# Performance work log

Hardware: AMD Instinct MI355X
Metric: run time of the kernel (lower is better)

## Reference

```python
import jax, jax.numpy as jnp
import numpy as np

EPS = 1e-5
K_NN = 16

def _lin1d(x, W, b):
    # 1x1 Conv1d: x (B,C,N) -> (B,O,N)
    return jnp.einsum('oc,bcn->bon', W, x) + b[None, :, None]

def _lin2d(x, W, b):
    # 1x1 Conv2d: x (B,C,N,K) -> (B,O,N,K)
    return jnp.einsum('oc,bcnk->bonk', W, x) + b[None, :, None, None]

def _bn2d(x, gamma, beta):
    # train-mode BatchNorm2d over (B, N, K) per channel
    mean = jnp.mean(x, axis=(0, 2, 3), keepdims=True)
    var = jnp.var(x, axis=(0, 2, 3), keepdims=True)
    xh = (x - mean) * jax.lax.rsqrt(var + EPS)
    return gamma[None, :, None, None] * xh + beta[None, :, None, None]

def _knn_idx(pq, ps, k):
    # pq (B,3,N), ps (B,3,M) -> idx (B,N,K) of k nearest support points
    d2 = (jnp.sum(pq * pq, axis=1)[:, :, None]
          + jnp.sum(ps * ps, axis=1)[:, None, :]
          - 2.0 * jnp.einsum('bcn,bcm->bnm', pq, ps))
    _, idx = jax.lax.top_k(-d2, k)
    return idx

def _group(x, idx):
    # x (B,C,M), idx (B,N,K) -> (B,C,N,K)
    return jnp.take_along_axis(x[:, :, None, :], idx[:, None, :, :], axis=3)

def setup_inputs() -> dict:
    key = jax.random.key(0)
    ks = jax.random.split(key, 20)
    B, C, D, N, M, H = 4, 128, 64, 2048, 2048, 256
    s = lambda k, shape, scale: (jax.random.normal(k, shape, dtype=jnp.float32) * scale)
    return {
        'pq': s(ks[0], (B, 3, N), 1.0),
        'fq': s(ks[1], (B, C, N), 1.0),
        'ps': s(ks[2], (B, 3, M), 1.0),
        'fs': s(ks[3], (B, C, M), 1.0),
        'Wq': s(ks[4], (D, C), 0.05), 'bq': jnp.zeros((D,), jnp.float32),
        'Wk': s(ks[5], (D, C), 0.05), 'bk': jnp.zeros((D,), jnp.float32),
        'Wv': s(ks[6], (D, C), 0.05), 'bv': jnp.zeros((D,), jnp.float32),
        'Wp1': s(ks[7], (D, 3), 0.2), 'bp1': jnp.zeros((D,), jnp.float32),
        'gp': jnp.ones((D,), jnp.float32), 'btp': jnp.zeros((D,), jnp.float32),
        'Wp2': s(ks[8], (D, D), 0.05), 'bp2': jnp.zeros((D,), jnp.float32),
        'Wa1': s(ks[9], (H, D), 0.05), 'ba1': jnp.zeros((H,), jnp.float32),
        'ga': jnp.ones((H,), jnp.float32), 'bta': jnp.zeros((H,), jnp.float32),
        'Wa2': s(ks[10], (D, H), 0.05), 'ba2': jnp.zeros((D,), jnp.float32),
        'We': s(ks[11], (C, D), 0.05), 'be': jnp.zeros((C,), jnp.float32),
    }

def reference(pq, fq, ps, fs, Wq, bq, Wk, bk, Wv, bv,
              Wp1, bp1, gp, btp, Wp2, bp2,
              Wa1, ba1, ga, bta, Wa2, ba2, We, be):
    identity = fq
    q = _lin1d(fq, Wq, bq)          # (B,D,N)
    k = _lin1d(fs, Wk, bk)          # (B,D,M)
    v = _lin1d(fs, Wv, bv)          # (B,D,M)
    idx = _knn_idx(pq, ps, K_NN)    # (B,N,K)
    key_g = _group(k, idx)          # (B,D,N,K)
    qk_rel = q[:, :, :, None] - key_g
    pos_rel = pq[:, :, :, None] - _group(ps, idx)  # (B,3,N,K)
    # pos_mlp: conv-bn-relu-conv
    pe = _lin2d(pos_rel, Wp1, bp1)
    pe = jax.nn.relu(_bn2d(pe, gp, btp))
    pe = _lin2d(pe, Wp2, bp2)       # (B,D,N,K)
    # attn_mlp: conv-bn-relu-conv
    a = _lin2d(qk_rel + pe, Wa1, ba1)
    a = jax.nn.relu(_bn2d(a, ga, bta))
    a = _lin2d(a, Wa2, ba2)         # (B,D,N,K)
    attn = jax.nn.softmax(a, axis=-1)
    val = _group(v, idx) + pe       # (B,D,N,K)
    agg = jnp.einsum('bcnk,bcnk->bcn', attn, val)
    return _lin1d(agg, We, be) + identity
```

## Files before the change

kernel.cpp:

```cpp
#include <hip/hip_runtime.h>
#include <stdint.h>

#define NN 2048
#define MM 2048
#define NSAMP 131072

typedef float  fv4 __attribute__((ext_vector_type(4)));
typedef short  bfv8 __attribute__((ext_vector_type(8)));
typedef short  bfv4 __attribute__((ext_vector_type(4)));
typedef unsigned short u16;
typedef unsigned long long u64;

__device__ inline u16 f2bf(float x){
  unsigned u = __float_as_uint(x);
  return (u16)((u + 0x7FFFu + ((u>>16)&1u)) >> 16);
}
__device__ inline float bf2f(u16 u){ return __uint_as_float(((unsigned)u)<<16); }
#define MFMA16 __builtin_amdgcn_mfma_f32_16x16x32_bf16

__global__ __launch_bounds__(256) void k_prep(
    const float* __restrict__ Wq, const float* __restrict__ Wk, const float* __restrict__ Wv,
    const float* __restrict__ Wp2, const float* __restrict__ Wa2, const float* __restrict__ We,
    const float* __restrict__ ps,
    u16* __restrict__ Wqbf, u16* __restrict__ Wkbf, u16* __restrict__ Wvbf,
    u16* __restrict__ Wp2bf, u16* __restrict__ Wa2bf, u16* __restrict__ Webf,
    fv4* __restrict__ psP) {
  int gid = blockIdx.x * 256 + threadIdx.x;
  if (gid < 8192)  { Wqbf[gid] = f2bf(Wq[gid]); Wkbf[gid] = f2bf(Wk[gid]);
                     Wvbf[gid] = f2bf(Wv[gid]); Webf[gid] = f2bf(We[gid]); }
  if (gid < 4096)  Wp2bf[gid] = f2bf(Wp2[gid]);
  if (gid < 16384) Wa2bf[gid] = f2bf(Wa2[gid]);
  if (gid < 8192)  { int b = gid >> 11, m = gid & 2047;
    float x = ps[(b*3+0)*MM + m], y = ps[(b*3+1)*MM + m], z = ps[(b*3+2)*MM + m];
    fv4 p; p.x = x; p.y = y; p.z = z; p.w = x*x + y*y + z*z;
    psP[gid] = p; }
}

__global__ __launch_bounds__(256) void k_qkv(
    const float* __restrict__ fq, const float* __restrict__ fs,
    const u16* __restrict__ Wqbf, const u16* __restrict__ Wkbf, const u16* __restrict__ Wvbf,
    const float* __restrict__ bq, const float* __restrict__ bk, const float* __restrict__ bv,
    float* __restrict__ qT, float* __restrict__ kT, float* __restrict__ vT) {
  __shared__ u16 tile[2][32 * 136];
  int bid = blockIdx.x;
  int b = bid >> 6, p0 = (bid & 63) * 32;
  int t = threadIdx.x;
  int w = t >> 6, l = t & 63, lq = l >> 4, ln = l & 15;
  {
    int cq = t >> 3, n4 = (t & 7) * 4;
    #pragma unroll
    for (int it = 0; it < 4; ++it) {
      int c = it * 32 + cq;
      fv4 vq = *(const fv4*)&fq[(b*128 + c)*2048 + p0 + n4];
      fv4 vs = *(const fv4*)&fs[(b*128 + c)*2048 + p0 + n4];
      #pragma unroll
      for (int j = 0; j < 4; ++j) {
        tile[0][(n4 + j)*136 + c] = f2bf(vq[j]);
        tile[1][(n4 + j)*136 + c] = f2bf(vs[j]);
      }
    }
  }
  bfv8 A[3][4];
  #pragma unroll
  for (int mat = 0; mat < 3; ++mat) {
    const u16* W = mat == 0 ? Wqbf : (mat == 1 ? Wkbf : Wvbf);
    #pragma unroll
    for (int kk = 0; kk < 4; ++kk)
      A[mat][kk] = *(const bfv8*)(W + (w*16 + ln)*128 + kk*32 + lq*8);
  }
  __syncthreads();
  fv4 acc[3][2];
  #pragma unroll
  for (int mat = 0; mat < 3; ++mat) {
    const u16* tl = tile[mat == 0 ? 0 : 1];
    #pragma unroll
    for (int nt = 0; nt < 2; ++nt) {
      fv4 a = {0.f,0.f,0.f,0.f};
      #pragma unroll
      for (int kk = 0; kk < 4; ++kk) {
        bfv8 bb = *(const bfv8*)&tl[(nt*16 + ln)*136 + kk*32 + lq*8];
        a = MFMA16(A[mat][kk], bb, a, 0, 0, 0);
      }
      acc[mat][nt] = a;
    }
  }
  #pragma unroll
  for (int mat = 0; mat < 3; ++mat) {
    float* dst = mat == 0 ? qT : (mat == 1 ? kT : vT);
    const float* bia = mat == 0 ? bq : (mat == 1 ? bk : bv);
    fv4 bq4 = *(const fv4*)&bia[w*16 + lq*4];
    #pragma unroll
    for (int nt = 0; nt < 2; ++nt) {
      fv4 o = acc[mat][nt] + bq4;
      *(fv4*)&dst[(b*NN + p0 + nt*16 + ln)*64 + w*16 + lq*4] = o;
    }
  }
}

__global__ __launch_bounds__(256) void k_knn(
    const float* __restrict__ pq, const fv4* __restrict__ psP,
    int* __restrict__ idxb, float* __restrict__ posPart) {
  __shared__ u64 list[4][512];
  __shared__ u64 win[4][16];
  __shared__ int cnt[4];
  __shared__ float sacc[4][9];

  const int t = threadIdx.x, w = t >> 6, lane = t & 63;
  const int qi = blockIdx.x * 4 + w;
  const int b = qi >> 11, n = qi & 2047;
  const float* pqb = pq + b * 3 * NN;
  const fv4* psb = psP + b * 2048;
  const float qx = pqb[n], qy = pqb[NN + n], qz = pqb[2 * NN + n];
  const float qq = qx * qx + qy * qy + qz * qz;

  unsigned key[32];
  unsigned bkey = 0xFFFFFFFFu; unsigned bj = 0;
  #pragma unroll
  for (int j = 0; j < 32; ++j) {
    fv4 P = psb[lane + 64*j];
    float d2 = qq + P.w - 2.f * (qx * P.x + qy * P.y + qz * P.z);
    unsigned bu = __float_as_uint(d2);
    bu = (bu & 0x80000000u) ? ~bu : (bu | 0x80000000u);
    key[j] = bu;
    if (bu < bkey) { bkey = bu; bj = (unsigned)j; }
  }
  u64 e = (((u64)bkey) << 32) | (unsigned)(lane + 64*(int)bj);

  #pragma unroll
  for (int k = 2; k <= 64; k <<= 1) {
    #pragma unroll
    for (int j = k >> 1; j > 0; j >>= 1) {
      u64 x = __shfl_xor(e, j, 64);
      u64 lo = e < x ? e : x, hi = e < x ? x : e;
      bool up = ((lane & k) == 0);
      bool takeLo = (((lane & j) == 0) == up);
      e = takeLo ? lo : hi;
    }
  }
  const u64 thr = __shfl(e, 15, 64);
  const unsigned T32 = (unsigned)(thr >> 32);

  if (lane == 0) cnt[w] = 0;
  #pragma unroll
  for (int j = 0; j < 32; ++j) {
    if (key[j] <= T32) {
      int p = atomicAdd(&cnt[w], 1);
      if (p < 512) list[w][p] = (((u64)key[j]) << 32) | (unsigned)(lane + 64*j);
    }
  }
  const int C = *(volatile int*)&cnt[w];

  u64 myWin = 0;
  if (C <= 64) {
    u64 v = (lane < C) ? list[w][lane] : ~0ULL;
    #pragma unroll
    for (int k = 2; k <= 64; k <<= 1) {
      #pragma unroll
      for (int j = k >> 1; j > 0; j >>= 1) {
        u64 x = __shfl_xor(v, j, 64);
        u64 lo = v < x ? v : x, hi = v < x ? x : v;
        bool up = ((lane & k) == 0);
        bool takeLo = (((lane & j) == 0) == up);
        v = takeLo ? lo : hi;
      }
    }
    myWin = v;
  } else if (C <= 128) {
    u64 e0 = list[w][lane];
    u64 e1 = (64 + lane < C) ? list[w][64 + lane] : ~0ULL;
    #pragma unroll
    for (unsigned k = 2; k <= 128; k <<= 1) {
      #pragma unroll
      for (unsigned j = k >> 1; j > 0; j >>= 1) {
        if (j < 64) {
          u64 x0 = __shfl_xor(e0, (int)j, 64);
          u64 x1 = __shfl_xor(e1, (int)j, 64);
          bool lower = ((lane & j) == 0);
          bool up0 = (k == 128) ? true : ((lane & k) == 0);
          bool up1 = (k == 128) ? true : ((k == 64) ? false : ((lane & k) == 0));
          e0 = (lower == up0) ? (e0 < x0 ? e0 : x0) : (e0 < x0 ? x0 : e0);
          e1 = (lower == up1) ? (e1 < x1 ? e1 : x1) : (e1 < x1 ? x1 : e1);
        } else {
          u64 lo = e0 < e1 ? e0 : e1, hi = e0 < e1 ? e1 : e0;
          e0 = lo; e1 = hi;
        }
      }
    }
    myWin = e0;
  } else {
    int Cc = C > 512 ? 512 : C;
    for (int i = lane; i < 512; i += 64)
      if (i >= Cc) list[w][i] = ~0ULL;
    for (int r = 0; r < 16; ++r) {
      u64 mv = ~0ULL;
      #pragma unroll
      for (int s5 = 0; s5 < 8; ++s5) {
        u64 x = list[w][s5*64 + lane];
        mv = x < mv ? x : mv;
      }
      #pragma unroll
      for (int off = 1; off <= 32; off <<= 1) {
        u64 x = __shfl_xor(mv, off, 64);
        mv = x < mv ? x : mv;
      }
      #pragma unroll
      for (int s5 = 0; s5 < 8; ++s5)
        if (list[w][s5*64 + lane] == mv) list[w][s5*64 + lane] = ~0ULL;
      if (lane == 0) win[w][r] = mv;
    }
    if (lane < 16) myWin = win[w][lane];
  }

  if (lane < 16) {
    unsigned m = (unsigned)(myWin & 0xFFFFFFFFu);
    idxb[qi * 16 + lane] = (int)m;
    fv4 P = psb[m];
    float r0 = qx - P.x, r1 = qy - P.y, r2 = qz - P.z;
    float s[9];
    s[0] = r0; s[1] = r1; s[2] = r2;
    s[3] = r0*r0; s[4] = r0*r1; s[5] = r0*r2;
    s[6] = r1*r1; s[7] = r1*r2; s[8] = r2*r2;
    #pragma unroll
    for (int off = 1; off <= 8; off <<= 1)
      #pragma unroll
      for (int i = 0; i < 9; ++i) s[i] += __shfl_xor(s[i], off, 64);
    if (lane == 0)
      #pragma unroll
      for (int i = 0; i < 9; ++i) sacc[w][i] = s[i];
  }
  __syncthreads();
  if (t < 9) posPart[blockIdx.x * 12 + t]
      = sacc[0][t] + sacc[1][t] + sacc[2][t] + sacc[3][t];
}

__global__ __launch_bounds__(256) void k_posfinal(
    const float* __restrict__ Wp1, const float* __restrict__ bp1,
    const float* __restrict__ gp, const float* __restrict__ btp,
    const float* __restrict__ posPart, float* __restrict__ Wp1f, float* __restrict__ bp1f) {
  __shared__ float red[4][9];
  __shared__ float st[9];
  int t = threadIdx.x;
  int w = t >> 6, lane = t & 63;
  float s[9];
  #pragma unroll
  for (int i = 0; i < 9; ++i) s[i] = 0.f;
  #pragma unroll
  for (int it = 0; it < 8; ++it) {
    const float* p = posPart + (it * 256 + t) * 12;
    fv4 a = *(const fv4*)p;
    fv4 b4 = *(const fv4*)(p + 4);
    float c8 = p[8];
    s[0]+=a.x; s[1]+=a.y; s[2]+=a.z; s[3]+=a.w;
    s[4]+=b4.x; s[5]+=b4.y; s[6]+=b4.z; s[7]+=b4.w;
    s[8]+=c8;
  }
  #pragma unroll
  for (int off = 32; off > 0; off >>= 1)
    #pragma unroll
    for (int i = 0; i < 9; ++i) s[i] += __shfl_xor(s[i], off, 64);
  if (lane == 0)
    #pragma unroll
    for (int i = 0; i < 9; ++i) red[w][i] = s[i];
  __syncthreads();
  if (t < 9) st[t] = red[0][t] + red[1][t] + red[2][t] + red[3][t];
  __syncthreads();
  if (t < 64) {
    int d = t;
    const float invN = 1.f / (float)NSAMP;
    float m0 = st[0]*invN, m1 = st[1]*invN, m2 = st[2]*invN;
    float C00 = st[3]*invN - m0*m0, C01 = st[4]*invN - m0*m1, C02 = st[5]*invN - m0*m2;
    float C11 = st[6]*invN - m1*m1, C12 = st[7]*invN - m1*m2, C22 = st[8]*invN - m2*m2;
    float w0 = Wp1[d*3], w1 = Wp1[d*3+1], w2 = Wp1[d*3+2];
    float mean = w0*m0 + w1*m1 + w2*m2 + bp1[d];
    float var = w0*w0*C00 + w1*w1*C11 + w2*w2*C22 + 2.f*(w0*w1*C01 + w0*w2*C02 + w1*w2*C12);
    float scale = gp[d] * rsqrtf(var + 1e-5f);
    Wp1f[d*3]   = scale * w0;
    Wp1f[d*3+1] = scale * w1;
    Wp1f[d*3+2] = scale * w2;
    bp1f[d] = btp[d] + scale * (bp1[d] - mean);
  }
}

__global__ __launch_bounds__(256) void k_ystats(
    const float* __restrict__ pq, const float* __restrict__ ps,
    const float* __restrict__ qT, const float* __restrict__ kT,
    const int* __restrict__ idxb,
    const float* __restrict__ Wp1f, const float* __restrict__ bp1f,
    const u16* __restrict__ Wp2bf, const float* __restrict__ bp2,
    float* __restrict__ Gpart, float* __restrict__ ySumPart) {
  __shared__ __align__(16) unsigned char smem[21760];
  u16*   hp   = (u16*)smem;
  u16*   y2   = (u16*)(smem + 9216);
  float* r3   = (float*)(smem + 18432);
  float* qc   = (float*)(smem + 19200);
  int*   idxA = (int*)(smem + 20224);
  float* sWp1 = (float*)(smem + 20480);
  float* sbp1 = (float*)(smem + 21248);
  float* sbp2 = (float*)(smem + 21504);

  const int t = threadIdx.x;
  const int w = t >> 6, l = t & 63, lq = l >> 4, ln = l & 15;
  const int d0 = 16*w + lq*4;

  if (t < 192) sWp1[t] = Wp1f[t];
  if (t < 64){ sbp1[t] = bp1f[t]; sbp2[t] = bp2[t]; }

  bfv8 Ape[2];
  #pragma unroll
  for (int kk = 0; kk < 2; ++kk)
    Ape[kk] = *(const bfv8*)(Wp2bf + (16*w + ln)*64 + kk*32 + lq*8);

  fv4 gacc[4];
  #pragma unroll
  for (int nt = 0; nt < 4; ++nt) gacc[nt] = (fv4){0.f,0.f,0.f,0.f};
  float ys[4] = {0.f, 0.f, 0.f, 0.f};
  __syncthreads();

  for (int ch = 0; ch < 2; ++ch) {
    const int p0 = blockIdx.x * 8 + ch * 4;
    const int b  = p0 >> 11;
    const int bN = b * 2048;
    if (t < 64) idxA[t] = idxb[p0*16 + t];
    qc[t] = qT[(p0 + (t>>6))*64 + (t & 63)];
    __syncthreads();
    if (t < 192) { int c = t >> 6, s = t & 63; int n = (p0 + (s>>4)) & 2047;
      r3[c*64 + s] = pq[(b*3+c)*NN + n] - ps[(b*3+c)*MM + idxA[s]]; }
    __syncthreads();
    { int s = t >> 2, iq = t & 3;
      float r0 = r3[s], r1 = r3[64+s], r2 = r3[128+s];
      u16 tmp[16];
      #pragma unroll
      for (int e = 0; e < 16; ++e) { int i = iq*16 + e;
        float v = sbp1[i] + sWp1[i*3]*r0 + sWp1[i*3+1]*r1 + sWp1[i*3+2]*r2;
        tmp[e] = f2bf(fmaxf(v, 0.f)); }
      *(bfv8*)&hp[s*72 + iq*16]     = *(const bfv8*)&tmp[0];
      *(bfv8*)&hp[s*72 + iq*16 + 8] = *(const bfv8*)&tmp[8];
    }
    __syncthreads();
    {
      fv4 pe[4];
      #pragma unroll
      for (int nt = 0; nt < 4; ++nt) {
        fv4 acc = {0.f,0.f,0.f,0.f};
        #pragma unroll
        for (int kk = 0; kk < 2; ++kk) {
          bfv8 bb = *(const bfv8*)&hp[(nt*16 + ln)*72 + kk*32 + lq*8];
          acc = MFMA16(Ape[kk], bb, acc, 0, 0, 0);
        }
        pe[nt] = acc;
      }
      fv4 bp2q = *(const fv4*)&sbp2[d0];
      #pragma unroll
      for (int nt = 0; nt < 4; ++nt) {
        int s = nt*16 + ln;
        int mi = idxA[s];
        fv4 kg = *(const fv4*)(kT + (bN + mi)*64 + d0);
        fv4 qv = *(const fv4*)&qc[nt*64 + d0];
        fv4 yv = qv - kg + pe[nt] + bp2q;
        #pragma unroll
        for (int r = 0; r < 4; ++r) { y2[(d0 + r)*72 + s] = f2bf(yv[r]); ys[r] += yv[r]; }
      }
    }
    __syncthreads();
    #pragma unroll
    for (int kk = 0; kk < 2; ++kk) {
      bfv8 aa = *(const bfv8*)&y2[(16*w + ln)*72 + kk*32 + lq*8];
      #pragma unroll
      for (int nt = 0; nt < 4; ++nt) {
        bfv8 bb = *(const bfv8*)&y2[(nt*16 + ln)*72 + kk*32 + lq*8];
        gacc[nt] = MFMA16(aa, bb, gacc[nt], 0, 0, 0);
      }
    }
    __syncthreads();
  }
  #pragma unroll
  for (int nt = 0; nt < 4; ++nt)
    #pragma unroll
    for (int r = 0; r < 4; ++r)
      Gpart[blockIdx.x*4096 + (16*w + lq*4 + r)*64 + nt*16 + ln] = gacc[nt][r];
  #pragma unroll
  for (int off = 1; off <= 8; off <<= 1) {
    #pragma unroll
    for (int r = 0; r < 4; ++r) ys[r] += __shfl_xor(ys[r], off, 64);
  }
  if (ln == 0) {
    #pragma unroll
    for (int r = 0; r < 4; ++r) ySumPart[blockIdx.x*64 + d0 + r] = ys[r];
  }
}

__global__ __launch_bounds__(256) void k_gred(
    const float* __restrict__ Gpart, const float* __restrict__ ySumPart,
    float* __restrict__ G, float* __restrict__ ySum) {
  __shared__ float red[256];
  int bid = blockIdx.x, t = threadIdx.x;
  int tj = t & 63, st = t >> 6;
  if (bid < 64) {
    int j = bid * 64 + tj;
    float s = 0.f;
    for (int p = st * 256; p < st * 256 + 256; ++p)
      s += Gpart[p*4096 + j];
    red[st * 64 + tj] = s;
    __syncthreads();
    if (t < 64)
      G[bid * 64 + t] = red[t] + red[64 + t] + red[128 + t] + red[192 + t];
  } else {
    float s = 0.f;
    for (int p = st * 256; p < st * 256 + 256; ++p)
      s += ySumPart[p*64 + tj];
    red[st * 64 + tj] = s;
    __syncthreads();
    if (t < 64)
      ySum[t] = red[t] + red[64 + t] + red[128 + t] + red[192 + t];
  }
}

__global__ __launch_bounds__(256) void k_attnfinal(
    const float* __restrict__ Wa1, const float* __restrict__ ba1,
    const float* __restrict__ ga, const float* __restrict__ bta,
    const float* __restrict__ ySum, const float* __restrict__ G,
    u16* __restrict__ Wa1fbf, float* __restrict__ ba1f) {
  __shared__ float red[256];
  __shared__ float mu[64];
  __shared__ float sc[1];
  int h = blockIdx.x, t = threadIdx.x;
  const float invN = 1.f / (float)NSAMP;
  if (t < 64) mu[t] = ySum[t] * invN;
  __syncthreads();
  float acc = 0.f;
  #pragma unroll
  for (int e = 0; e < 16; ++e) {
    int pi = t*16 + e, i = pi >> 6, j = pi & 63;
    float cov = G[pi]*invN - mu[i]*mu[j];
    acc += Wa1[h*64 + i] * Wa1[h*64 + j] * cov;
  }
  red[t] = acc;
  __syncthreads();
  for (int s = 128; s > 0; s >>= 1) { if (t < s) red[t] += red[t + s]; __syncthreads(); }
  float var = red[0];
  __syncthreads();
  red[t] = (t < 64) ? Wa1[h*64 + t] * mu[t] : 0.f;
  __syncthreads();
  for (int s = 128; s > 0; s >>= 1) { if (t < s) red[t] += red[t + s]; __syncthreads(); }
  if (t == 0) {
    float mean  = red[0] + ba1[h];
    float scale = ga[h] * rsqrtf(var + 1e-5f);
    sc[0] = scale;
    ba1f[h] = bta[h] + scale * (ba1[h] - mean);
  }
  __syncthreads();
  if (t < 64) Wa1fbf[h*64 + t] = f2bf(sc[0] * Wa1[h*64 + t]);
}

__global__ __launch_bounds__(256, 4) void k_main(
    const float* __restrict__ pq, const float* __restrict__ ps,
    const float* __restrict__ qT, const float* __restrict__ kT, const float* __restrict__ vT,
    const int* __restrict__ idxb,
    const float* __restrict__ Wp1f, const float* __restrict__ bp1f,
    const u16* __restrict__ Wp2bf, const float* __restrict__ bp2,
    const u16* __restrict__ Wa1fbf, const float* __restrict__ ba1f,
    const u16* __restrict__ Wa2bf, const float* __restrict__ ba2,
    u16* __restrict__ aggbf) {
  __shared__ __align__(16) unsigned char smem[37120];
  u16*   hp   = (u16*)smem;
  u16*   ylds = (u16*)(smem + 9216);
  u16*   ha   = (u16*)smem;
  float* r3   = (float*)(smem + 33792);
  float* qc   = (float*)(smem + 34560);
  int*   idxA = (int*)(smem + 35584);
  float* sWp1 = (float*)(smem + 35840);
  float* sbp1 = (float*)(smem + 36608);
  float* sbp2 = (float*)(smem + 36864);

  const int t = threadIdx.x;
  const int w = t >> 6, l = t & 63, lq = l >> 4, ln = l & 15;
  const int d0 = 16*w + lq*4;
  const int p0 = blockIdx.x * 4;
  const int b  = p0 >> 11;
  const int bN = b * 2048;

  if (t < 192) sWp1[t] = Wp1f[t];
  if (t < 64){ sbp1[t] = bp1f[t]; sbp2[t] = bp2[t]; }
  if (t < 64) idxA[t] = idxb[p0*16 + t];
  qc[t] = qT[(p0 + (t>>6))*64 + (t & 63)];
  __syncthreads();

  if (t < 192) { int c = t >> 6, s = t & 63; int n = (p0 + (s>>4)) & 2047;
    r3[c*64 + s] = pq[(b*3+c)*NN + n] - ps[(b*3+c)*MM + idxA[s]]; }
  __syncthreads();

  { int s = t >> 2, iq = t & 3;
    float r0 = r3[s], r1 = r3[64+s], r2 = r3[128+s];
    u16 tmp[16];
    #pragma unroll
    for (int e = 0; e < 16; ++e) { int i = iq*16 + e;
      float v = sbp1[i] + sWp1[i*3]*r0 + sWp1[i*3+1]*r1 + sWp1[i*3+2]*r2;
      tmp[e] = f2bf(fmaxf(v, 0.f)); }
    *(bfv8*)&hp[s*72 + iq*16]     = *(const bfv8*)&tmp[0];
    *(bfv8*)&hp[s*72 + iq*16 + 8] = *(const bfv8*)&tmp[8];
  }
  __syncthreads();

  u16 vp[4][4];
  {
    bfv8 Ape[2];
    #pragma unroll
    for (int kk = 0; kk < 2; ++kk)
      Ape[kk] = *(const bfv8*)(Wp2bf + (16*w + ln)*64 + kk*32 + lq*8);
    fv4 pe[4];
    #pragma unroll
    for (int nt = 0; nt < 4; ++nt) {
      fv4 acc = {0.f,0.f,0.f,0.f};
      #pragma unroll
      for (int kk = 0; kk < 2; ++kk) {
        bfv8 bb = *(const bfv8*)&hp[(nt*16 + ln)*72 + kk*32 + lq*8];
        acc = MFMA16(Ape[kk], bb, acc, 0, 0, 0);
      }
      pe[nt] = acc;
    }
    fv4 bp2q = *(const fv4*)&sbp2[d0];
    #pragma unroll
    for (int nt = 0; nt < 4; ++nt) {
      int s = nt*16 + ln;
      int mi = idxA[s];
      fv4 kg = *(const fv4*)(kT + (bN + mi)*64 + d0);
      fv4 vg = *(const fv4*)(vT + (bN + mi)*64 + d0);
      fv4 qv = *(const fv4*)&qc[nt*64 + d0];
      fv4 pv = pe[nt] + bp2q;
      fv4 yv = qv - kg + pv;
      fv4 vv = vg + pv;
      u16 yp[4];
      #pragma unroll
      for (int r = 0; r < 4; ++r) { yp[r] = f2bf(yv[r]); vp[nt][r] = f2bf(vv[r]); }
      *(bfv4*)&ylds[s*72 + d0] = *(const bfv4*)yp;
    }
  }
  __syncthreads();

  bfv8 yb0[4], yb1[4];
  #pragma unroll
  for (int nt = 0; nt < 4; ++nt) {
    int s = nt*16 + ln;
    yb0[nt] = *(const bfv8*)&ylds[s*72 + lq*8];
    yb1[nt] = *(const bfv8*)&ylds[s*72 + 32 + lq*8];
  }
  __syncthreads();

  {
    bfv8 A1[4][2];
    #pragma unroll
    for (int mt = 0; mt < 4; ++mt)
      #pragma unroll
      for (int kk = 0; kk < 2; ++kk)
        A1[mt][kk] = *(const bfv8*)(Wa1fbf + (64*w + mt*16 + ln)*64 + kk*32 + lq*8);
    #pragma unroll
    for (int nt = 0; nt < 4; ++nt) {
      int s = nt*16 + ln;
      #pragma unroll
      for (int mt = 0; mt < 4; ++mt) {
        fv4 acc = {0.f,0.f,0.f,0.f};
        acc = MFMA16(A1[mt][0], yb0[nt], acc, 0, 0, 0);
        acc = MFMA16(A1[mt][1], yb1[nt], acc, 0, 0, 0);
        int h0 = 64*w + mt*16 + lq*4;
        fv4 bq = *(const fv4*)&ba1f[h0];
        u16 hv[4];
        #pragma unroll
        for (int r = 0; r < 4; ++r) hv[r] = f2bf(fmaxf(acc[r] + bq[r], 0.f));
        *(bfv4*)&ha[s*264 + h0] = *(const bfv4*)hv;
      }
    }
  }
  __syncthreads();

  fv4 acc2[4];
  #pragma unroll
  for (int nt = 0; nt < 4; ++nt) acc2[nt] = (fv4){0.f,0.f,0.f,0.f};
  {
    #pragma unroll
    for (int kk = 0; kk < 8; ++kk) {
      bfv8 A2 = *(const bfv8*)(Wa2bf + (16*w + ln)*256 + kk*32 + lq*8);
      #pragma unroll
      for (int nt = 0; nt < 4; ++nt) {
        bfv8 bb = *(const bfv8*)&ha[(nt*16 + ln)*264 + kk*32 + lq*8];
        acc2[nt] = MFMA16(A2, bb, acc2[nt], 0, 0, 0);
      }
    }
  }
  const fv4 ba2q = *(const fv4*)&ba2[d0];
  #pragma unroll
  for (int nt = 0; nt < 4; ++nt) {
    fv4 a = acc2[nt] + ba2q;
    fv4 m = a;
    #pragma unroll
    for (int off = 1; off <= 8; off <<= 1)
      #pragma unroll
      for (int r = 0; r < 4; ++r) m[r] = fmaxf(m[r], __shfl_xor(m[r], off, 16));
    fv4 ee, num;
    #pragma unroll
    for (int r = 0; r < 4; ++r) {
      ee[r] = __expf(a[r] - m[r]);
      num[r] = ee[r] * bf2f(vp[nt][r]);
    }
    fv4 sum = ee;
    #pragma unroll
    for (int off = 1; off <= 8; off <<= 1)
      #pragma unroll
      for (int r = 0; r < 4; ++r) {
        sum[r] += __shfl_xor(sum[r], off, 16);
        num[r] += __shfl_xor(num[r], off, 16);
      }
    if (ln == 0) {
      u16 o[4];
      #pragma unroll
      for (int r = 0; r < 4; ++r) o[r] = f2bf(num[r] / sum[r]);
      *(bfv4*)&aggbf[(u64)(p0 + nt)*64 + d0] = *(const bfv4*)o;
    }
  }
}

__global__ __launch_bounds__(256) void k_epi(
    const u16* __restrict__ aggbf, const u16* __restrict__ Webf,
    const float* __restrict__ be, const float* __restrict__ fq,
    float* __restrict__ out) {
  const int t = threadIdx.x;
  const int w = t >> 6, l = t & 63, lq = l >> 4, ln = l & 15;
  const int P0 = blockIdx.x * 16;
  const int b  = P0 >> 11;
  const int n0 = P0 & 2047;
  bfv8 EA[2][2];
  #pragma unroll
  for (int mt = 0; mt < 2; ++mt)
    #pragma unroll
    for (int kk = 0; kk < 2; ++kk)
      EA[mt][kk] = *(const bfv8*)(Webf + ((w*2 + mt)*16 + ln)*64 + kk*32 + lq*8);
  const u16* bp = aggbf + (P0 + ln)*64;
  bfv8 b0 = *(const bfv8*)(bp + lq*8);
  bfv8 b1 = *(const bfv8*)(bp + 32 + lq*8);
  fv4 eacc[2];
  #pragma unroll
  for (int mt = 0; mt < 2; ++mt) {
    fv4 a = {0.f,0.f,0.f,0.f};
    a = MFMA16(EA[mt][0], b0, a, 0, 0, 0);
    a = MFMA16(EA[mt][1], b1, a, 0, 0, 0);
    eacc[mt] = a;
  }
  #pragma unroll
  for (int mt = 0; mt < 2; ++mt) {
    int c0 = (w*2 + mt)*16 + lq*4;
    fv4 bev = *(const fv4*)&be[c0];
    #pragma unroll
    for (int r = 0; r < 4; ++r) {
      int c = c0 + r;
      int o = (b*128 + c)*2048 + n0 + ln;
      out[o] = eacc[mt][r] + bev[r] + fq[o];
    }
  }
}

extern "C" void kernel_launch(void* const* d_in, const int* in_sizes, int n_in,
                              void* d_out, int out_size, void* d_ws, size_t ws_size,
                              hipStream_t stream) {
  (void)in_sizes; (void)n_in; (void)out_size; (void)ws_size;
  const float* pq  = (const float*)d_in[0];
  const float* fq  = (const float*)d_in[1];
  const float* ps  = (const float*)d_in[2];
  const float* fs  = (const float*)d_in[3];
  const float* Wq  = (const float*)d_in[4];  const float* bq  = (const float*)d_in[5];
  const float* Wk  = (const float*)d_in[6];  const float* bk  = (const float*)d_in[7];
  const float* Wv  = (const float*)d_in[8];  const float* bv  = (const float*)d_in[9];
  const float* Wp1 = (const float*)d_in[10]; const float* bp1 = (const float*)d_in[11];
  const float* gp  = (const float*)d_in[12]; const float* btp = (const float*)d_in[13];
  const float* Wp2 = (const float*)d_in[14]; const float* bp2 = (const float*)d_in[15];
  const float* Wa1 = (const float*)d_in[16]; const float* ba1 = (const float*)d_in[17];
  const float* ga  = (const float*)d_in[18]; const float* bta = (const float*)d_in[19];
  const float* Wa2 = (const float*)d_in[20]; const float* ba2 = (const float*)d_in[21];
  const float* We  = (const float*)d_in[22]; const float* be  = (const float*)d_in[23];
  float* ws = (float*)d_ws;
  float* qT    = ws;
  float* kT    = ws + 524288;
  float* vT    = ws + 1048576;
  u16*   aggbf = (u16*)(ws + 1572864);
  int*   idxb  = (int*)(ws + 1835008);
  u16*   Wqbf  = (u16*)(ws + 1966080);
  u16*   Wkbf  = (u16*)(ws + 1970176);
  u16*   Wvbf  = (u16*)(ws + 1974272);
  u16*   Webf  = (u16*)(ws + 1978368);
  fv4*   psP   = (fv4*)(ws + 1982464);
  float* Wp1f  = ws + 2015232;
  float* bp1f  = ws + 2015424;
  float* ba1f  = ws + 2015488;
  float* G     = ws + 2015744;
  float* ySum  = ws + 2019840;
  float* ySumP = ws + 2019904;
  u16*   Wp2bf  = (u16*)(ws + 2085440);
  u16*   Wa2bf  = (u16*)(ws + 2087488);
  u16*   Wa1fbf = (u16*)(ws + 2095680);
  float* posPart = ws + 2103872;
  float* Gpart   = ws + 2128448;
  float* out   = (float*)d_out;

  k_prep<<<64, 256, 0, stream>>>(Wq, Wk, Wv, Wp2, Wa2, We, ps,
                                 Wqbf, Wkbf, Wvbf, Wp2bf, Wa2bf, Webf, psP);
  k_qkv<<<256, 256, 0, stream>>>(fq, fs, Wqbf, Wkbf, Wvbf, bq, bk, bv, qT, kT, vT);
  k_knn<<<2048, 256, 0, stream>>>(pq, psP, idxb, posPart);
  k_posfinal<<<1, 256, 0, stream>>>(Wp1, bp1, gp, btp, posPart, Wp1f, bp1f);
  k_ystats<<<1024, 256, 0, stream>>>(pq, ps, qT, kT, idxb, Wp1f, bp1f, Wp2bf, bp2,
                                     Gpart, ySumP);
  k_gred<<<65, 256, 0, stream>>>(Gpart, ySumP, G, ySum);
  k_attnfinal<<<256, 256, 0, stream>>>(Wa1, ba1, ga, bta, ySum, G, Wa1fbf, ba1f);
  k_main<<<2048, 256, 0, stream>>>(pq, ps, qT, kT, vT, idxb, Wp1f, bp1f, Wp2bf, bp2,
                                   Wa1fbf, ba1f, Wa2bf, ba2, aggbf);
  k_epi<<<512, 256, 0, stream>>>(aggbf, Webf, be, fq, out);
}
```

Baseline: 229.9 us.

## Fuse epilogue projection into main attention kernel with per-block point loop

The main kernel now handles 16 points per block in a loop of four 4-point chunks. It keeps the attention aggregate in shared memory and applies the output projection plus residual directly, so the separate epilogue kernel and the global agg buffer are gone. Weight fragments (Wp2, Wa1, biases) are loaded into registers once per block and reused across the chunks. In exchange the grid shrinks to 512 blocks, shared memory grows, and launch bounds drop to 3 blocks per SM, which lowers occupancy and parallelism.

```diff
diff --git a/kernel.cpp b/kernel.cpp
--- a/kernel.cpp
+++ b/kernel.cpp
@@ -452,7 +452,7 @@
   if (t < 64) Wa1fbf[h*64 + t] = f2bf(sc[0] * Wa1[h*64 + t]);
 }
 
-__global__ __launch_bounds__(256, 4) void k_main(
+__global__ __launch_bounds__(256, 3) void k_main(
     const float* __restrict__ pq, const float* __restrict__ ps,
     const float* __restrict__ qT, const float* __restrict__ kT, const float* __restrict__ vT,
     const int* __restrict__ idxb,
@@ -460,122 +460,117 @@
     const u16* __restrict__ Wp2bf, const float* __restrict__ bp2,
     const u16* __restrict__ Wa1fbf, const float* __restrict__ ba1f,
     const u16* __restrict__ Wa2bf, const float* __restrict__ ba2,
-    u16* __restrict__ aggbf) {
-  __shared__ __align__(16) unsigned char smem[37120];
+    const u16* __restrict__ Webf, const float* __restrict__ be,
+    const float* __restrict__ fq,
+    float* __restrict__ out) {
+  __shared__ __align__(16) unsigned char smem[48640];
   u16*   hp   = (u16*)smem;
-  u16*   ylds = (u16*)(smem + 9216);
   u16*   ha   = (u16*)smem;
-  float* r3   = (float*)(smem + 33792);
-  float* qc   = (float*)(smem + 34560);
-  int*   idxA = (int*)(smem + 35584);
-  float* sWp1 = (float*)(smem + 35840);
-  float* sbp1 = (float*)(smem + 36608);
-  float* sbp2 = (float*)(smem + 36864);
+  u16*   ylds = (u16*)(smem + 33792);
+  float* r3   = (float*)(smem + 43008);
+  float* qc   = (float*)(smem + 43776);
+  int*   idxA = (int*)(smem + 44800);
+  float* sWp1 = (float*)(smem + 45056);
+  float* sbp1 = (float*)(smem + 45824);
+  u16*   aggL = (u16*)(smem + 46336);
 
   const int t = threadIdx.x;
   const int w = t >> 6, l = t & 63, lq = l >> 4, ln = l & 15;
   const int d0 = 16*w + lq*4;
-  const int p0 = blockIdx.x * 4;
-  const int b  = p0 >> 11;
+  const int P0 = blockIdx.x * 16;
+  const int b  = P0 >> 11;
   const int bN = b * 2048;
 
   if (t < 192) sWp1[t] = Wp1f[t];
-  if (t < 64){ sbp1[t] = bp1f[t]; sbp2[t] = bp2[t]; }
-  if (t < 64) idxA[t] = idxb[p0*16 + t];
-  qc[t] = qT[(p0 + (t>>6))*64 + (t & 63)];
-  __syncthreads();
-
-  if (t < 192) { int c = t >> 6, s = t & 63; int n = (p0 + (s>>4)) & 2047;
-    r3[c*64 + s] = pq[(b*3+c)*NN + n] - ps[(b*3+c)*MM + idxA[s]]; }
-  __syncthreads();
-
-  { int s = t >> 2, iq = t & 3;
-    float r0 = r3[s], r1 = r3[64+s], r2 = r3[128+s];
-    u16 tmp[16];
-    #pragma unroll
-    for (int e = 0; e < 16; ++e) { int i = iq*16 + e;
-      float v = sbp1[i] + sWp1[i*3]*r0 + sWp1[i*3+1]*r1 + sWp1[i*3+2]*r2;
-      tmp[e] = f2bf(fmaxf(v, 0.f)); }
-    *(bfv8*)&hp[s*72 + iq*16]     = *(const bfv8*)&tmp[0];
-    *(bfv8*)&hp[s*72 + iq*16 + 8] = *(const bfv8*)&tmp[8];
-  }
-  __syncthreads();
-
-  u16 vp[4][4];
-  {
-    bfv8 Ape[2];
+  if (t < 64) sbp1[t] = bp1f[t];
+
+  bfv8 Ape[2], A1[4][2];
+  #pragma unroll
+  for (int kk = 0; kk < 2; ++kk)
+    Ape[kk] = *(const bfv8*)(Wp2bf + (16*w + ln)*64 + kk*32 + lq*8);
+  #pragma unroll
+  for (int mt = 0; mt < 4; ++mt)
     #pragma unroll
     for (int kk = 0; kk < 2; ++kk)
-      Ape[kk] = *(const bfv8*)(Wp2bf + (16*w + ln)*64 + kk*32 + lq*8);
-    fv4 pe[4];
-    #pragma unroll
-    for (int nt = 0; nt < 4; ++nt) {
-      fv4 acc = {0.f,0.f,0.f,0.f};
-      #pragma unroll
-      for (int kk = 0; kk < 2; ++kk) {
-        bfv8 bb = *(const bfv8*)&hp[(nt*16 + ln)*72 + kk*32 + lq*8];
-        acc = MFMA16(Ape[kk], bb, acc, 0, 0, 0);
-      }
-      pe[nt] = acc;
-    }
-    fv4 bp2q = *(const fv4*)&sbp2[d0];
+      A1[mt][kk] = *(const bfv8*)(Wa1fbf + (64*w + mt*16 + ln)*64 + kk*32 + lq*8);
+  fv4 bq1[4];
+  #pragma unroll
+  for (int mt = 0; mt < 4; ++mt)
+    bq1[mt] = *(const fv4*)&ba1f[64*w + mt*16 + lq*4];
+  const fv4 ba2q = *(const fv4*)&ba2[d0];
+  const fv4 bp2q = *(const fv4*)&bp2[d0];
+
+  for (int ch = 0; ch < 4; ++ch) {
+    const int p0 = P0 + ch * 4;
+    if (t < 64) idxA[t] = idxb[p0*16 + t];
+    qc[t] = qT[(p0 + (t>>6))*64 + (t & 63)];
+    __syncthreads();
+    if (t < 192) { int c = t >> 6, s = t & 63; int n = (p0 + (s>>4)) & 2047;
+      r3[c*64 + s] = pq[(b*3+c)*NN + n] - ps[(b*3+c)*MM + idxA[s]]; }
+    __syncthreads();
+    { int s = t >> 2, iq = t & 3;
+      float r0 = r3[s], r1 = r3[64+s], r2 = r3[128+s];
+      u16 tmp[16];
+      #pragma unroll
+      for (int e = 0; e < 16; ++e) { int i = iq*16 + e;
+        float v = sbp1[i] + sWp1[i*3]*r0 + sWp1[i*3+1]*r1 + sWp1[i*3+2]*r2;
+        tmp[e] = f2bf(fmaxf(v, 0.f)); }
+      *(bfv8*)&hp[s*72 + iq*16]     = *(const bfv8*)&tmp[0];
+      *(bfv8*)&hp[s*72 + iq*16 + 8] = *(const bfv8*)&tmp[8];
+    }
+    __syncthreads();
+    u16 vp[4][4];
+    {
+      fv4 pe[4];
+      #pragma unroll
+      for (int nt = 0; nt < 4; ++nt) {
+        fv4 acc = {0.f,0.f,0.f,0.f};
+        #pragma unroll
+        for (int kk = 0; kk < 2; ++kk) {
+          bfv8 bb = *(const bfv8*)&hp[(nt*16 + ln)*72 + kk*32 + lq*8];
+          acc = MFMA16(Ape[kk], bb, acc, 0, 0, 0);
+        }
+        pe[nt] = acc;
+      }
+      #pragma unroll
+      for (int nt = 0; nt < 4; ++nt) {
+        int s = nt*16 + ln;
+        int mi = idxA[s];
+        fv4 kg = *(const fv4*)(kT + (bN + mi)*64 + d0);
+        fv4 vg = *(const fv4*)(vT + (bN + mi)*64 + d0);
+        fv4 qv = *(const fv4*)&qc[nt*64 + d0];
+        fv4 pv = pe[nt] + bp2q;
+        fv4 yv = qv - kg + pv;
+        fv4 vv = vg + pv;
+        u16 yp[4];
+        #pragma unroll
+        for (int r = 0; r < 4; ++r) { yp[r] = f2bf(yv[r]); vp[nt][r] = f2bf(vv[r]); }
+        *(bfv4*)&ylds[s*72 + d0] = *(const bfv4*)yp;
+      }
+    }
+    __syncthreads();
     #pragma unroll
     for (int nt = 0; nt < 4; ++nt) {
       int s = nt*16 + ln;
-      int mi = idxA[s];
-      fv4 kg = *(const fv4*)(kT + (bN + mi)*64 + d0);
-      fv4 vg = *(const fv4*)(vT + (bN + mi)*64 + d0);
-      fv4 qv = *(const fv4*)&qc[nt*64 + d0];
-      fv4 pv = pe[nt] + bp2q;
-      fv4 yv = qv - kg + pv;
-      fv4 vv = vg + pv;
-      u16 yp[4];
-      #pragma unroll
-      for (int r = 0; r < 4; ++r) { yp[r] = f2bf(yv[r]); vp[nt][r] = f2bf(vv[r]); }
-      *(bfv4*)&ylds[s*72 + d0] = *(const bfv4*)yp;
-    }
-  }
-  __syncthreads();
-
-  bfv8 yb0[4], yb1[4];
-  #pragma unroll
-  for (int nt = 0; nt < 4; ++nt) {
-    int s = nt*16 + ln;
-    yb0[nt] = *(const bfv8*)&ylds[s*72 + lq*8];
-    yb1[nt] = *(const bfv8*)&ylds[s*72 + 32 + lq*8];
-  }
-  __syncthreads();
-
-  {
-    bfv8 A1[4][2];
-    #pragma unroll
-    for (int mt = 0; mt < 4; ++mt)
-      #pragma unroll
-      for (int kk = 0; kk < 2; ++kk)
-        A1[mt][kk] = *(const bfv8*)(Wa1fbf + (64*w + mt*16 + ln)*64 + kk*32 + lq*8);
-    #pragma unroll
-    for (int nt = 0; nt < 4; ++nt) {
-      int s = nt*16 + ln;
+      bfv8 yb0 = *(const bfv8*)&ylds[s*72 + lq*8];
+      bfv8 yb1 = *(const bfv8*)&ylds[s*72 + 32 + lq*8];
       #pragma unroll
       for (int mt = 0; mt < 4; ++mt) {
         fv4 acc = {0.f,0.f,0.f,0.f};
-        acc = MFMA16(A1[mt][0], yb0[nt], acc, 0, 0, 0);
-        acc = MFMA16(A1[mt][1], yb1[nt], acc, 0, 0, 0);
+        acc = MFMA16(A1[mt][0], yb0, acc, 0, 0, 0);
+        acc = MFMA16(A1[mt][1], yb1, acc, 0, 0, 0);
         int h0 = 64*w + mt*16 + lq*4;
-        fv4 bq = *(const fv4*)&ba1f[h0];
+        fv4 bq = bq1[mt];
         u16 hv[4];
         #pragma unroll
         for (int r = 0; r < 4; ++r) hv[r] = f2bf(fmaxf(acc[r] + bq[r], 0.f));
         *(bfv4*)&ha[s*264 + h0] = *(const bfv4*)hv;
       }
     }
-  }
-  __syncthreads();
-
-  fv4 acc2[4];
-  #pragma unroll
-  for (int nt = 0; nt < 4; ++nt) acc2[nt] = (fv4){0.f,0.f,0.f,0.f};
-  {
+    __syncthreads();
+    fv4 acc2[4];
+    #pragma unroll
+    for (int nt = 0; nt < 4; ++nt) acc2[nt] = (fv4){0.f,0.f,0.f,0.f};
     #pragma unroll
     for (int kk = 0; kk < 8; ++kk) {
       bfv8 A2 = *(const bfv8*)(Wa2bf + (16*w + ln)*256 + kk*32 + lq*8);
@@ -585,74 +580,66 @@
         acc2[nt] = MFMA16(A2, bb, acc2[nt], 0, 0, 0);
       }
     }
-  }
-  const fv4 ba2q = *(const fv4*)&ba2[d0];
-  #pragma unroll
-  for (int nt = 0; nt < 4; ++nt) {
-    fv4 a = acc2[nt] + ba2q;
-    fv4 m = a;
-    #pragma unroll
-    for (int off = 1; off <= 8; off <<= 1)
-      #pragma unroll
-      for (int r = 0; r < 4; ++r) m[r] = fmaxf(m[r], __shfl_xor(m[r], off, 16));
-    fv4 ee, num;
-    #pragma unroll
-    for (int r = 0; r < 4; ++r) {
-      ee[r] = __expf(a[r] - m[r]);
-      num[r] = ee[r] * bf2f(vp[nt][r]);
-    }
-    fv4 sum = ee;
-    #pragma unroll
-    for (int off = 1; off <= 8; off <<= 1)
+    #pragma unroll
+    for (int nt = 0; nt < 4; ++nt) {
+      fv4 a = acc2[nt] + ba2q;
+      fv4 m = a;
+      #pragma unroll
+      for (int off = 1; off <= 8; off <<= 1)
+        #pragma unroll
+        for (int r = 0; r < 4; ++r) m[r] = fmaxf(m[r], __shfl_xor(m[r], off, 16));
+      fv4 ee, num;
       #pragma unroll
       for (int r = 0; r < 4; ++r) {
-        sum[r] += __shfl_xor(sum[r], off, 16);
-        num[r] += __shfl_xor(num[r], off, 16);
-      }
-    if (ln == 0) {
-      u16 o[4];
-      #pragma unroll
-      for (int r = 0; r < 4; ++r) o[r] = f2bf(num[r] / sum[r]);
-      *(bfv4*)&aggbf[(u64)(p0 + nt)*64 + d0] = *(const bfv4*)o;
-    }
-  }
-}
-
-__global__ __launch_bounds__(256) void k_epi(
-    const u16* __restrict__ aggbf, const u16* __restrict__ Webf,
-    const float* __restrict__ be, const float* __restrict__ fq,
-    float* __restrict__ out) {
-  const int t = threadIdx.x;
-  const int w = t >> 6, l = t & 63, lq = l >> 4, ln = l & 15;
-  const int P0 = blockIdx.x * 16;
-  const int b  = P0 >> 11;
-  const int n0 = P0 & 2047;
-  bfv8 EA[2][2];
-  #pragma unroll
-  for (int mt = 0; mt < 2; ++mt)
-    #pragma unroll
-    for (int kk = 0; kk < 2; ++kk)
-      EA[mt][kk] = *(const bfv8*)(Webf + ((w*2 + mt)*16 + ln)*64 + kk*32 + lq*8);
-  const u16* bp = aggbf + (P0 + ln)*64;
-  bfv8 b0 = *(const bfv8*)(bp + lq*8);
-  bfv8 b1 = *(const bfv8*)(bp + 32 + lq*8);
-  fv4 eacc[2];
-  #pragma unroll
-  for (int mt = 0; mt < 2; ++mt) {
-    fv4 a = {0.f,0.f,0.f,0.f};
-    a = MFMA16(EA[mt][0], b0, a, 0, 0, 0);
-    a = MFMA16(EA[mt][1], b1, a, 0, 0, 0);
-    eacc[mt] = a;
-  }
-  #pragma unroll
-  for (int mt = 0; mt < 2; ++mt) {
-    int c0 = (w*2 + mt)*16 + lq*4;
-    fv4 bev = *(const fv4*)&be[c0];
-    #pragma unroll
-    for (int r = 0; r < 4; ++r) {
-      int c = c0 + r;
-      int o = (b*128 + c)*2048 + n0 + ln;
-      out[o] = eacc[mt][r] + bev[r] + fq[o];
+        ee[r] = __expf(a[r] - m[r]);
+        num[r] = ee[r] * bf2f(vp[nt][r]);
+      }
+      fv4 sum = ee;
+      #pragma unroll
+      for (int off = 1; off <= 8; off <<= 1)
+        #pragma unroll
+        for (int r = 0; r < 4; ++r) {
+          sum[r] += __shfl_xor(sum[r], off, 16);
+          num[r] += __shfl_xor(num[r], off, 16);
+        }
+      if (ln == 0) {
+        u16 o[4];
+        #pragma unroll
+        for (int r = 0; r < 4; ++r) o[r] = f2bf(num[r] / sum[r]);
+        *(bfv4*)&aggL[(ch*4 + nt)*72 + d0] = *(const bfv4*)o;
+      }
+    }
+    __syncthreads();
+  }
+  {
+    const int n0 = P0 & 2047;
+    bfv8 EA[2][2];
+    #pragma unroll
+    for (int mt = 0; mt < 2; ++mt)
+      #pragma unroll
+      for (int kk = 0; kk < 2; ++kk)
+        EA[mt][kk] = *(const bfv8*)(Webf + ((w*2 + mt)*16 + ln)*64 + kk*32 + lq*8);
+    const u16* bp = aggL + ln*72;
+    bfv8 b0 = *(const bfv8*)(bp + lq*8);
+    bfv8 b1 = *(const bfv8*)(bp + 32 + lq*8);
+    fv4 eacc[2];
+    #pragma unroll
+    for (int mt = 0; mt < 2; ++mt) {
+      fv4 a = {0.f,0.f,0.f,0.f};
+      a = MFMA16(EA[mt][0], b0, a, 0, 0, 0);
+      a = MFMA16(EA[mt][1], b1, a, 0, 0, 0);
+      eacc[mt] = a;
+    }
+    #pragma unroll
+    for (int mt = 0; mt < 2; ++mt) {
+      int c0 = (w*2 + mt)*16 + lq*4;
+      fv4 bev = *(const fv4*)&be[c0];
+      #pragma unroll
+      for (int r = 0; r < 4; ++r) {
+        int c = c0 + r;
+        int o = (b*128 + c)*2048 + n0 + ln;
+        out[o] = eacc[mt][r] + bev[r] + fq[o];
+      }
     }
   }
 }
@@ -679,7 +666,6 @@
   float* qT    = ws;
   float* kT    = ws + 524288;
   float* vT    = ws + 1048576;
-  u16*   aggbf = (u16*)(ws + 1572864);
   int*   idxb  = (int*)(ws + 1835008);
   u16*   Wqbf  = (u16*)(ws + 1966080);
   u16*   Wkbf  = (u16*)(ws + 1970176);
@@ -708,7 +694,6 @@
                                      Gpart, ySumP);
   k_gred<<<65, 256, 0, stream>>>(Gpart, ySumP, G, ySum);
   k_attnfinal<<<256, 256, 0, stream>>>(Wa1, ba1, ga, bta, ySum, G, Wa1fbf, ba1f);
-  k_main<<<2048, 256, 0, stream>>>(pq, ps, qT, kT, vT, idxb, Wp1f, bp1f, Wp2bf, bp2,
-                                   Wa1fbf, ba1f, Wa2bf, ba2, aggbf);
-  k_epi<<<512, 256, 0, stream>>>(aggbf, Webf, be, fq, out);
-}
+  k_main<<<512, 256, 0, stream>>>(pq, ps, qT, kT, vT, idxb, Wp1f, bp1f, Wp2bf, bp2,
+                                  Wa1fbf, ba1f, Wa2bf, ba2, Webf, be, fq, out);
+}
```

Result: no change. 233.5 us (+1.6%).
